# Kernel tuning notes

Hardware: AMD Instinct MI355X
Metric: run time of the kernel (lower is better)

Reference implementation:

```python
import jax, jax.numpy as jnp
import numpy as np

D_MODEL = 1024
N_HEADS = 16
HEAD_DIM = D_MODEL // N_HEADS


def setup_inputs() -> dict:
    key = jax.random.key(0)
    k1, k2, k3 = jax.random.split(key, 3)
    B, T = 2, 2048
    x = jax.random.normal(k1, (B, T, D_MODEL), dtype=jnp.float32)
    # causal lower-triangular mask; positions with mask==0 are blocked
    mask = jnp.tril(jnp.ones((T, T), dtype=jnp.int32))
    s = 1.0 / np.sqrt(D_MODEL)
    W_qkv = jax.random.normal(k2, (D_MODEL, 3 * D_MODEL), dtype=jnp.float32) * s
    W_out = jax.random.normal(k3, (D_MODEL, D_MODEL), dtype=jnp.float32) * s
    return {"x": x, "mask": mask, "W_qkv": W_qkv, "W_out": W_out}


def reference(x, mask, W_qkv, W_out):
    B, T, C = x.shape
    qkv = x @ W_qkv  # [B, T, 3C]
    q, k, v = jnp.split(qkv, 3, axis=-1)
    # [B, H, T, Dh]
    def heads(t):
        return t.reshape(B, T, N_HEADS, HEAD_DIM).transpose(0, 2, 1, 3)
    q, k, v = heads(q), heads(k), heads(v)
    scale = jnp.float32(1.0 / np.sqrt(HEAD_DIM))
    attn = jnp.einsum("bhqd,bhkd->bhqk", q, k) * scale  # [B,H,T,T]
    attn = jnp.where(mask == 0, jnp.float32(-jnp.inf), attn)
    attn = jax.nn.softmax(attn, axis=-1)
    out = jnp.einsum("bhqk,bhkd->bhqd", attn, v)  # [B,H,T,Dh]
    out = out.transpose(0, 2, 1, 3).reshape(B, T, C)
    return out @ W_out
```

## Files before the change

### kernel.cpp

```cpp
#include <hip/hip_runtime.h>
#include <hip/hip_bf16.h>

typedef __bf16 bf16;
typedef __bf16 bf16x4 __attribute__((ext_vector_type(4)));
typedef __bf16 bf16x8 __attribute__((ext_vector_type(8)));
typedef float f32x4 __attribute__((ext_vector_type(4)));
typedef float f32x16 __attribute__((ext_vector_type(16)));
typedef unsigned int uint4v __attribute__((ext_vector_type(4)));

__device__ __forceinline__ void gld_lds16(const void* g, void* l) {
  __builtin_amdgcn_global_load_lds(
      (const __attribute__((address_space(1))) void*)g,
      (__attribute__((address_space(3))) void*)l, 16, 0, 0);
}

__device__ __forceinline__ unsigned pkbf(float a, float b) {
  union { bf16 h[2]; unsigned u; } x;
  x.h[0] = (bf16)a; x.h[1] = (bf16)b;
  return x.u;
}

__device__ __forceinline__ void plswap2(unsigned& a, unsigned& b) {
  asm volatile("" : "+v"(a), "+v"(b));
  asm("v_permlane32_swap_b32 %0, %1" : "+v"(a), "+v"(b));
}

__device__ __forceinline__ float asf(unsigned u) { return __builtin_bit_cast(float, u); }

__device__ __forceinline__ float plsum(float x) {
  unsigned a = __builtin_bit_cast(unsigned, x), b = a;
  plswap2(a, b);
  return asf(a) + asf(b);
}

__global__ __launch_bounds__(256) void cvt_kernel(const float* __restrict__ src,
                                                  bf16* __restrict__ dst, int n4) {
  int i = blockIdx.x * 256 + threadIdx.x;
  if (i < n4) {
    float4 v = ((const float4*)src)[i];
    bf16x4 o = { (bf16)v.x, (bf16)v.y, (bf16)v.z, (bf16)v.w };
    ((bf16x4*)dst)[i] = o;
  }
}

__global__ __launch_bounds__(256) void transpose_cvt_kernel(const float* __restrict__ src,
                                                            bf16* __restrict__ dst,
                                                            int R, int C) {
  __shared__ float tile[32][33];
  int tx = threadIdx.x & 31, ty = threadIdx.x >> 5;
  int bx = blockIdx.x * 32, by = blockIdx.y * 32;
#pragma unroll
  for (int j = 0; j < 32; j += 8)
    tile[ty + j][tx] = src[(size_t)(by + ty + j) * C + bx + tx];
  __syncthreads();
#pragma unroll
  for (int j = 0; j < 32; j += 8)
    dst[(size_t)(bx + ty + j) * R + by + tx] = (bf16)tile[tx][ty + j];
}

__global__ __launch_bounds__(256) void transpose_v_kernel(const bf16* __restrict__ src,
                                                          bf16* __restrict__ dst) {
  __shared__ bf16 tile[32][34];
  int bh = blockIdx.z;
  int t0 = blockIdx.x * 32;
  int d0 = blockIdx.y * 32;
  int tx = threadIdx.x & 31, ty = threadIdx.x >> 5;
  const bf16* s = src + (size_t)bh * 2048 * 64;
  bf16* d = dst + (size_t)bh * 64 * 2048;
#pragma unroll
  for (int j = 0; j < 32; j += 8)
    tile[ty + j][tx] = s[(size_t)(t0 + ty + j) * 64 + d0 + tx];
  __syncthreads();
#pragma unroll
  for (int j = 0; j < 32; j += 8)
    d[(size_t)(d0 + ty + j) * 2048 + t0 + tx] = tile[tx][ty + j];
}

template <int MODE>
__global__ __launch_bounds__(256) void gemm_kernel(
    const bf16* __restrict__ A, const bf16* __restrict__ BT,
    float* __restrict__ Cf, bf16* __restrict__ qb, bf16* __restrict__ kb,
    bf16* __restrict__ vb, int M, int N, int K) {
  __shared__ bf16 As[128 * 64];
  __shared__ bf16 Bs[128 * 64];
  const int t = threadIdx.x;
  const int w = t >> 6, l = t & 63;

  int wid = blockIdx.y * gridDim.x + blockIdx.x;
  int cpx = (gridDim.x * gridDim.y) >> 3;
  int swz = (wid & 7) * cpx + (wid >> 3);
  const int bm = (swz / gridDim.x) * 128, bn = (swz % gridDim.x) * 128;

  const int wr = (w >> 1) * 64, wc = (w & 1) * 64;
  const int lr = l & 15, lh = l >> 4;
  f32x4 acc[4][4] = {};

  const bf16* Ab = A + (size_t)bm * K;
  const bf16* Bb = BT + (size_t)bn * K;
  char* AsB = (char*)As;
  char* BsB = (char*)Bs;

  const int srow_ = t >> 3;
  const int scol = (((t & 7) * 16) ^ ((srow_ & 7) << 4)) >> 1;
  const int ldsw = w * 1024;

  for (int k0 = 0; k0 < K; k0 += 64) {
    __syncthreads();
#pragma unroll
    for (int c = 0; c < 4; ++c) {
      const int row = c * 32 + srow_;
      gld_lds16(Ab + (size_t)row * K + k0 + scol, AsB + c * 4096 + ldsw);
      gld_lds16(Bb + (size_t)row * K + k0 + scol, BsB + c * 4096 + ldsw);
    }
    __syncthreads();
#pragma unroll
    for (int kk = 0; kk < 2; ++kk) {
      bf16x8 af[4], bfr[4];
#pragma unroll
      for (int m = 0; m < 4; ++m) {
        const int R = wr + m * 16 + lr;
        af[m] = *(const bf16x8*)(AsB + R * 128 + ((kk * 64 + lh * 16) ^ ((R & 7) << 4)));
      }
#pragma unroll
      for (int n = 0; n < 4; ++n) {
        const int R = wc + n * 16 + lr;
        bfr[n] = *(const bf16x8*)(BsB + R * 128 + ((kk * 64 + lh * 16) ^ ((R & 7) << 4)));
      }
#pragma unroll
      for (int m = 0; m < 4; ++m)
#pragma unroll
        for (int n = 0; n < 4; ++n)
          acc[m][n] = __builtin_amdgcn_mfma_f32_16x16x32_bf16(af[m], bfr[n],
                                                              acc[m][n], 0, 0, 0);
    }
  }

  const int r0 = bm + wr + (lh << 2);
  const int c0 = bn + wc + lr;
#pragma unroll
  for (int m = 0; m < 4; ++m) {
#pragma unroll
    for (int n = 0; n < 4; ++n) {
#pragma unroll
      for (int r = 0; r < 4; ++r) {
        float v = acc[m][n][r];
        int row = r0 + m * 16 + r;
        int col = c0 + n * 16;
        if (MODE == 2) {
          Cf[(size_t)row * N + col] = v;
        } else {
          int bb = row >> 11, tt = row & 2047;
          if (col < 1024) {
            int h = col >> 6, d = col & 63;
            qb[(((size_t)(bb * 16 + h)) * 2048 + tt) * 64 + d] = (bf16)v;
          } else if (col < 2048) {
            int c = col - 1024, h = c >> 6, d = c & 63;
            kb[(((size_t)(bb * 16 + h)) * 2048 + tt) * 64 + d] = (bf16)v;
          } else {
            int c = col - 2048, h = c >> 6, d = c & 63;
            vb[(((size_t)(bb * 16 + h)) * 2048 + tt) * 64 + d] = (bf16)v;
          }
        }
      }
    }
  }
}

template <bool FLIP>
__device__ __forceinline__ void attn_main(const bf16* __restrict__ Qh,
                                          const bf16* __restrict__ Kh,
                                          const bf16* __restrict__ Vh,
                                          bf16* __restrict__ ao,
                                          int qw, int lastkt, int l,
                                          int bb, int h, bf16 (*pl)[72]) {
  const int lq = l & 31, hi = l >> 5;
  const float sc2 = 0.125f * 1.4426950408889634f;

  bf16x8 qf[4];
#pragma unroll
  for (int c = 0; c < 4; ++c)
    qf[c] = *(const bf16x8*)(Qh + (size_t)(qw + lq) * 64 + c * 16 + hi * 8);

  f32x16 Ot0, Ot1;
#pragma unroll
  for (int r = 0; r < 16; ++r) { Ot0[r] = 0.f; Ot1[r] = 0.f; }
  float srun = 0.f;

  bf16x8 kA[4], vA[4], kB[4], vB[4];
#pragma unroll
  for (int c = 0; c < 4; ++c)
    kA[c] = *(const bf16x8*)(Kh + (size_t)lq * 64 + c * 16 + hi * 8);
#pragma unroll
  for (int df = 0; df < 2; ++df)
#pragma unroll
    for (int c = 0; c < 2; ++c)
      vA[df * 2 + c] = *(const bf16x8*)(Vh + (size_t)(df * 32 + lq) * 2048 + c * 16 + hi * 8);

  auto step = [&](bf16x8 (&KC)[4], bf16x8 (&VC)[4],
                  bf16x8 (&KN)[4], bf16x8 (&VN)[4], int kt) {
    const int nkv0 = (kt << 5) + 32;
#pragma unroll
    for (int c = 0; c < 4; ++c)
      KN[c] = *(const bf16x8*)(Kh + (size_t)(nkv0 + lq) * 64 + c * 16 + hi * 8);
#pragma unroll
    for (int df = 0; df < 2; ++df)
#pragma unroll
      for (int c = 0; c < 2; ++c)
        VN[df * 2 + c] = *(const bf16x8*)(Vh + (size_t)(df * 32 + lq) * 2048 + nkv0 + c * 16 + hi * 8);

    f32x16 S;
#pragma unroll
    for (int r = 0; r < 16; ++r) S[r] = 0.f;
#pragma unroll
    for (int c = 0; c < 4; ++c)
      S = __builtin_amdgcn_mfma_f32_32x32x16_bf16(KC[c], qf[c], S, 0, 0, 0);

    if (kt == lastkt) {
#pragma unroll
      for (int r = 0; r < 16; ++r) {
        int kvl = (r & 3) + 8 * (r >> 2) + 4 * hi;
        if (kvl > lq) S[r] = -1e30f;
      }
    }

    float ps = 0.f;
    unsigned u_[8];
#pragma unroll
    for (int i = 0; i < 8; ++i) {
      float pa = exp2f(S[2 * i] * sc2);
      float pb = exp2f(S[2 * i + 1] * sc2);
      ps += pa + pb;
      u_[i] = pkbf(pa, pb);
    }
    srun += plsum(ps);

    unsigned a0 = u_[0], b0 = u_[2]; plswap2(a0, b0);
    unsigned a1 = u_[1], b1 = u_[3]; plswap2(a1, b1);
    unsigned a2 = u_[4], b2 = u_[6]; plswap2(a2, b2);
    unsigned a3 = u_[5], b3 = u_[7]; plswap2(a3, b3);
    uint4v f0, f1;
    if (FLIP) { f0 = (uint4v){b0, b1, a0, a1}; f1 = (uint4v){b2, b3, a2, a3}; }
    else      { f0 = (uint4v){a0, a1, b0, b1}; f1 = (uint4v){a2, a3, b2, b3}; }
    bf16x8 pf0 = __builtin_bit_cast(bf16x8, f0);
    bf16x8 pf1 = __builtin_bit_cast(bf16x8, f1);

    Ot0 = __builtin_amdgcn_mfma_f32_32x32x16_bf16(VC[0], pf0, Ot0, 0, 0, 0);
    Ot0 = __builtin_amdgcn_mfma_f32_32x32x16_bf16(VC[1], pf1, Ot0, 0, 0, 0);
    Ot1 = __builtin_amdgcn_mfma_f32_32x32x16_bf16(VC[2], pf0, Ot1, 0, 0, 0);
    Ot1 = __builtin_amdgcn_mfma_f32_32x32x16_bf16(VC[3], pf1, Ot1, 0, 0, 0);
  };

  for (int kt = 0; kt <= lastkt; ++kt) {
    if ((kt & 1) == 0) step(kA, vA, kB, vB, kt);
    else               step(kB, vB, kA, vA, kt);
  }

  float inv = 1.0f / srun;
#pragma unroll
  for (int r = 0; r < 16; r += 2) {
    int d0 = (r & 3) + 8 * (r >> 2) + 4 * hi;
    *(unsigned*)&pl[lq][d0]      = pkbf(Ot0[r] * inv, Ot0[r + 1] * inv);
    *(unsigned*)&pl[lq][32 + d0] = pkbf(Ot1[r] * inv, Ot1[r + 1] * inv);
  }
  __builtin_amdgcn_s_waitcnt(0);

  const int q = l >> 1, dh = (l & 1) * 32;
  size_t orow = ((size_t)(bb * 2048 + qw + q)) * 1024 + h * 64 + dh;
#pragma unroll
  for (int c = 0; c < 4; ++c) {
    bf16x8 vv = *(const bf16x8*)&pl[q][dh + c * 8];
    *(bf16x8*)(ao + orow + c * 8) = vv;
  }
}

__global__ __launch_bounds__(512, 2) void attn_kernel(const bf16* __restrict__ qb,
                                                      const bf16* __restrict__ kb,
                                                      const bf16* __restrict__ vt,
                                                      bf16* __restrict__ ao) {
  __shared__ bf16 plds[8][32][72];
  int wid = blockIdx.y * 8 + blockIdx.x;
  int swz = (wid & 7) * 32 + (wid >> 3);
  const int bh = swz >> 3;
  const int grp = swz & 7;
  const int w = threadIdx.x >> 6, l = threadIdx.x & 63;
  const int jj = grp * 4 + (w & 3);
  const int qc = (w >> 2) ? (63 - jj) : jj;
  const bf16* Qh = qb + (size_t)bh * 2048 * 64;
  const bf16* Kh = kb + (size_t)bh * 2048 * 64;
  const bf16* Vh = vt + (size_t)bh * 64 * 2048;

  unsigned ta = (unsigned)l, tb = (unsigned)l;
  plswap2(ta, tb);
  const bool flipped = (ta != (unsigned)(l & 31));

  if (flipped)
    attn_main<true>(Qh, Kh, Vh, ao, qc * 32, qc, l, bh >> 4, bh & 15, plds[w]);
  else
    attn_main<false>(Qh, Kh, Vh, ao, qc * 32, qc, l, bh >> 4, bh & 15, plds[w]);
}

extern "C" void kernel_launch(void* const* d_in, const int* in_sizes, int n_in,
                              void* d_out, int out_size, void* d_ws, size_t ws_size,
                              hipStream_t stream) {
  const float* x = (const float*)d_in[0];
  const float* Wqkv = (const float*)d_in[2];
  const float* Wout = (const float*)d_in[3];
  float* out = (float*)d_out;

  char* ws = (char*)d_ws;
  bf16* xb  = (bf16*)(ws);
  bf16* wqT = (bf16*)(ws + (size_t)(8 << 20));
  bf16* woT = (bf16*)(ws + (size_t)(14 << 20));
  bf16* qb  = (bf16*)(ws + (size_t)(16 << 20));
  bf16* kb  = (bf16*)(ws + (size_t)(24 << 20));
  bf16* vt  = (bf16*)(ws + (size_t)(32 << 20));
  bf16* ao  = (bf16*)(ws + (size_t)(40 << 20));
  bf16* vb  = (bf16*)(ws + (size_t)(48 << 20));

  cvt_kernel<<<dim3(4096), dim3(256), 0, stream>>>(x, xb, 1048576);
  transpose_cvt_kernel<<<dim3(96, 32), dim3(256), 0, stream>>>(Wqkv, wqT, 1024, 3072);
  transpose_cvt_kernel<<<dim3(32, 32), dim3(256), 0, stream>>>(Wout, woT, 1024, 1024);
  gemm_kernel<1><<<dim3(24, 32), dim3(256), 0, stream>>>(xb, wqT, nullptr, qb, kb, vb,
                                                         4096, 3072, 1024);
  transpose_v_kernel<<<dim3(64, 2, 32), dim3(256), 0, stream>>>(vb, vt);
  attn_kernel<<<dim3(8, 32), dim3(512), 0, stream>>>(qb, kb, vt, ao);
  gemm_kernel<2><<<dim3(8, 32), dim3(256), 0, stream>>>(ao, woT, out, nullptr, nullptr,
                                                        nullptr, 4096, 1024, 1024);
}
```

Before: 219.3 us.

## Process two KV tiles per attention step with raw v_exp and MFMA priority

The attention inner loop now handles 64 keys per iteration, as two 32-key tiles, instead of 32. K for the next pair is prefetched into registers, while V is loaded at the start of the current step rather than one step ahead. The causal mask logic is rewritten to cover the two-tile pair, exp2f is replaced with inline v_exp_f32, and MFMA sections are wrapped in s_setprio. The aim is more instruction-level parallelism and fewer loop iterations, at the cost of higher register pressure and V loads that are exposed within the step.

```diff
diff --git a/kernel.cpp b/kernel.cpp
--- a/kernel.cpp
+++ b/kernel.cpp
@@ -18,6 +18,12 @@
   union { bf16 h[2]; unsigned u; } x;
   x.h[0] = (bf16)a; x.h[1] = (bf16)b;
   return x.u;
+}
+
+__device__ __forceinline__ float exp2r(float x) {
+  float r;
+  asm("v_exp_f32 %0, %1" : "=v"(r) : "v"(x));
+  return r;
 }
 
 __device__ __forceinline__ void plswap2(unsigned& a, unsigned& b) {
@@ -171,7 +177,7 @@
                                           const bf16* __restrict__ Kh,
                                           const bf16* __restrict__ Vh,
                                           bf16* __restrict__ ao,
-                                          int qw, int lastkt, int l,
+                                          int qw, int qc, int l,
                                           int bb, int h, bf16 (*pl)[72]) {
   const int lq = l & 31, hi = l >> 5;
   const float sc2 = 0.125f * 1.4426950408889634f;
@@ -186,73 +192,112 @@
   for (int r = 0; r < 16; ++r) { Ot0[r] = 0.f; Ot1[r] = 0.f; }
   float srun = 0.f;
 
-  bf16x8 kA[4], vA[4], kB[4], vB[4];
-#pragma unroll
-  for (int c = 0; c < 4; ++c)
-    kA[c] = *(const bf16x8*)(Kh + (size_t)lq * 64 + c * 16 + hi * 8);
-#pragma unroll
-  for (int df = 0; df < 2; ++df)
-#pragma unroll
-    for (int c = 0; c < 2; ++c)
-      vA[df * 2 + c] = *(const bf16x8*)(Vh + (size_t)(df * 32 + lq) * 2048 + c * 16 + hi * 8);
-
-  auto step = [&](bf16x8 (&KC)[4], bf16x8 (&VC)[4],
-                  bf16x8 (&KN)[4], bf16x8 (&VN)[4], int kt) {
-    const int nkv0 = (kt << 5) + 32;
+  bf16x8 kA[8], kB[8], vC[8];
+#pragma unroll
+  for (int tc = 0; tc < 8; ++tc)
+    kA[tc] = *(const bf16x8*)(Kh + (size_t)((tc >> 2) * 32 + lq) * 64 + (tc & 3) * 16 + hi * 8);
+
+  const int lastp = qc >> 1;
+
+  auto step = [&](bf16x8 (&KC)[8], bf16x8 (&KN)[8], int p) {
+    const int kv0 = p << 6;
+    const int nkv = kv0 + 64;
+#pragma unroll
+    for (int tc = 0; tc < 8; ++tc)
+      KN[tc] = *(const bf16x8*)(Kh + (size_t)(nkv + (tc >> 2) * 32 + lq) * 64 + (tc & 3) * 16 + hi * 8);
+#pragma unroll
+    for (int t = 0; t < 2; ++t)
+#pragma unroll
+      for (int df = 0; df < 2; ++df)
+#pragma unroll
+        for (int c = 0; c < 2; ++c)
+          vC[t * 4 + df * 2 + c] =
+              *(const bf16x8*)(Vh + (size_t)(df * 32 + lq) * 2048 + kv0 + t * 32 + c * 16 + hi * 8);
+
+    f32x16 S0, S1;
+#pragma unroll
+    for (int r = 0; r < 16; ++r) { S0[r] = 0.f; S1[r] = 0.f; }
+    __builtin_amdgcn_s_setprio(1);
 #pragma unroll
     for (int c = 0; c < 4; ++c)
-      KN[c] = *(const bf16x8*)(Kh + (size_t)(nkv0 + lq) * 64 + c * 16 + hi * 8);
-#pragma unroll
-    for (int df = 0; df < 2; ++df)
-#pragma unroll
-      for (int c = 0; c < 2; ++c)
-        VN[df * 2 + c] = *(const bf16x8*)(Vh + (size_t)(df * 32 + lq) * 2048 + nkv0 + c * 16 + hi * 8);
-
-    f32x16 S;
-#pragma unroll
-    for (int r = 0; r < 16; ++r) S[r] = 0.f;
+      S0 = __builtin_amdgcn_mfma_f32_32x32x16_bf16(KC[c], qf[c], S0, 0, 0, 0);
 #pragma unroll
     for (int c = 0; c < 4; ++c)
-      S = __builtin_amdgcn_mfma_f32_32x32x16_bf16(KC[c], qf[c], S, 0, 0, 0);
-
-    if (kt == lastkt) {
-#pragma unroll
-      for (int r = 0; r < 16; ++r) {
-        int kvl = (r & 3) + 8 * (r >> 2) + 4 * hi;
-        if (kvl > lq) S[r] = -1e30f;
+      S1 = __builtin_amdgcn_mfma_f32_32x32x16_bf16(KC[4 + c], qf[c], S1, 0, 0, 0);
+    __builtin_amdgcn_s_setprio(0);
+
+    const int t0 = 2 * p, t1 = 2 * p + 1;
+    if (t1 >= qc) {
+      if (t0 == qc) {
+#pragma unroll
+        for (int r = 0; r < 16; ++r) {
+          int kvl = (r & 3) + 8 * (r >> 2) + 4 * hi;
+          if (kvl > lq) S0[r] = -1e30f;
+          S1[r] = -1e30f;
+        }
+      } else {
+#pragma unroll
+        for (int r = 0; r < 16; ++r) {
+          int kvl = (r & 3) + 8 * (r >> 2) + 4 * hi;
+          if (kvl > lq) S1[r] = -1e30f;
+        }
       }
     }
 
-    float ps = 0.f;
-    unsigned u_[8];
+    float ps0 = 0.f, ps1 = 0.f;
+    unsigned u0_[8], u1_[8];
 #pragma unroll
     for (int i = 0; i < 8; ++i) {
-      float pa = exp2f(S[2 * i] * sc2);
-      float pb = exp2f(S[2 * i + 1] * sc2);
-      ps += pa + pb;
-      u_[i] = pkbf(pa, pb);
-    }
-    srun += plsum(ps);
-
-    unsigned a0 = u_[0], b0 = u_[2]; plswap2(a0, b0);
-    unsigned a1 = u_[1], b1 = u_[3]; plswap2(a1, b1);
-    unsigned a2 = u_[4], b2 = u_[6]; plswap2(a2, b2);
-    unsigned a3 = u_[5], b3 = u_[7]; plswap2(a3, b3);
-    uint4v f0, f1;
-    if (FLIP) { f0 = (uint4v){b0, b1, a0, a1}; f1 = (uint4v){b2, b3, a2, a3}; }
-    else      { f0 = (uint4v){a0, a1, b0, b1}; f1 = (uint4v){a2, a3, b2, b3}; }
-    bf16x8 pf0 = __builtin_bit_cast(bf16x8, f0);
-    bf16x8 pf1 = __builtin_bit_cast(bf16x8, f1);
-
-    Ot0 = __builtin_amdgcn_mfma_f32_32x32x16_bf16(VC[0], pf0, Ot0, 0, 0, 0);
-    Ot0 = __builtin_amdgcn_mfma_f32_32x32x16_bf16(VC[1], pf1, Ot0, 0, 0, 0);
-    Ot1 = __builtin_amdgcn_mfma_f32_32x32x16_bf16(VC[2], pf0, Ot1, 0, 0, 0);
-    Ot1 = __builtin_amdgcn_mfma_f32_32x32x16_bf16(VC[3], pf1, Ot1, 0, 0, 0);
+      float a = exp2r(S0[2 * i] * sc2);
+      float b = exp2r(S0[2 * i + 1] * sc2);
+      ps0 += a + b;
+      u0_[i] = pkbf(a, b);
+    }
+#pragma unroll
+    for (int i = 0; i < 8; ++i) {
+      float a = exp2r(S1[2 * i] * sc2);
+      float b = exp2r(S1[2 * i + 1] * sc2);
+      ps1 += a + b;
+      u1_[i] = pkbf(a, b);
+    }
+    srun += plsum(ps0 + ps1);
+
+    unsigned a0 = u0_[0], b0 = u0_[2]; plswap2(a0, b0);
+    unsigned a1 = u0_[1], b1 = u0_[3]; plswap2(a1, b1);
+    unsigned a2 = u0_[4], b2 = u0_[6]; plswap2(a2, b2);
+    unsigned a3 = u0_[5], b3 = u0_[7]; plswap2(a3, b3);
+    unsigned c0 = u1_[0], d0 = u1_[2]; plswap2(c0, d0);
+    unsigned c1 = u1_[1], d1 = u1_[3]; plswap2(c1, d1);
+    unsigned c2 = u1_[4], d2 = u1_[6]; plswap2(c2, d2);
+    unsigned c3 = u1_[5], d3 = u1_[7]; plswap2(c3, d3);
+    uint4v f00, f01, f10, f11;
+    if (FLIP) {
+      f00 = (uint4v){b0, b1, a0, a1}; f01 = (uint4v){b2, b3, a2, a3};
+      f10 = (uint4v){d0, d1, c0, c1}; f11 = (uint4v){d2, d3, c2, c3};
+    } else {
+      f00 = (uint4v){a0, a1, b0, b1}; f01 = (uint4v){a2, a3, b2, b3};
+      f10 = (uint4v){c0, c1, d0, d1}; f11 = (uint4v){c2, c3, d2, d3};
+    }
+    bf16x8 p00 = __builtin_bit_cast(bf16x8, f00);
+    bf16x8 p01 = __builtin_bit_cast(bf16x8, f01);
+    bf16x8 p10 = __builtin_bit_cast(bf16x8, f10);
+    bf16x8 p11 = __builtin_bit_cast(bf16x8, f11);
+
+    __builtin_amdgcn_s_setprio(1);
+    Ot0 = __builtin_amdgcn_mfma_f32_32x32x16_bf16(vC[0], p00, Ot0, 0, 0, 0);
+    Ot0 = __builtin_amdgcn_mfma_f32_32x32x16_bf16(vC[1], p01, Ot0, 0, 0, 0);
+    Ot1 = __builtin_amdgcn_mfma_f32_32x32x16_bf16(vC[2], p00, Ot1, 0, 0, 0);
+    Ot1 = __builtin_amdgcn_mfma_f32_32x32x16_bf16(vC[3], p01, Ot1, 0, 0, 0);
+    Ot0 = __builtin_amdgcn_mfma_f32_32x32x16_bf16(vC[4], p10, Ot0, 0, 0, 0);
+    Ot0 = __builtin_amdgcn_mfma_f32_32x32x16_bf16(vC[5], p11, Ot0, 0, 0, 0);
+    Ot1 = __builtin_amdgcn_mfma_f32_32x32x16_bf16(vC[6], p10, Ot1, 0, 0, 0);
+    Ot1 = __builtin_amdgcn_mfma_f32_32x32x16_bf16(vC[7], p11, Ot1, 0, 0, 0);
+    __builtin_amdgcn_s_setprio(0);
   };
 
-  for (int kt = 0; kt <= lastkt; ++kt) {
-    if ((kt & 1) == 0) step(kA, vA, kB, vB, kt);
-    else               step(kB, vB, kA, vA, kt);
+  for (int p = 0; p <= lastp; ++p) {
+    if ((p & 1) == 0) step(kA, kB, p);
+    else              step(kB, kA, p);
   }
 
   float inv = 1.0f / srun;
```

Measured after the change: 233.5 us. 6.5% more time.

## Software-pipeline QK^T one tile ahead of softmax/PV in attention loop

Applied to the files above, without the earlier changes.

Restructures the causal attention inner loop so the QK^T MFMA for the next key tile is issued before the exp/PV work of the current tile. K loads move two tiles ahead and V loads one tile ahead. It also brackets the MFMA groups with s_setprio and replaces exp2f with a raw v_exp_f32 inline asm. The aim is to overlap matrix-core work with the VALU exponentials and hide load latency, at the cost of more live registers. The final iteration computes an extra QK tile and issues loads past the causal range that are never used.

```diff
diff --git a/kernel.cpp b/kernel.cpp
--- a/kernel.cpp
+++ b/kernel.cpp
@@ -18,6 +18,12 @@
   union { bf16 h[2]; unsigned u; } x;
   x.h[0] = (bf16)a; x.h[1] = (bf16)b;
   return x.u;
+}
+
+__device__ __forceinline__ float exp2r(float x) {
+  float r;
+  asm("v_exp_f32 %0, %1" : "=v"(r) : "v"(x));
+  return r;
 }
 
 __device__ __forceinline__ void plswap2(unsigned& a, unsigned& b) {
@@ -171,7 +177,7 @@
                                           const bf16* __restrict__ Kh,
                                           const bf16* __restrict__ Vh,
                                           bf16* __restrict__ ao,
-                                          int qw, int lastkt, int l,
+                                          int qw, int qc, int l,
                                           int bb, int h, bf16 (*pl)[72]) {
   const int lq = l & 31, hi = l >> 5;
   const float sc2 = 0.125f * 1.4426950408889634f;
@@ -181,12 +187,12 @@
   for (int c = 0; c < 4; ++c)
     qf[c] = *(const bf16x8*)(Qh + (size_t)(qw + lq) * 64 + c * 16 + hi * 8);
 
-  f32x16 Ot0, Ot1;
+  f32x16 Ot0, Ot1, Sa, Sb;
 #pragma unroll
   for (int r = 0; r < 16; ++r) { Ot0[r] = 0.f; Ot1[r] = 0.f; }
   float srun = 0.f;
 
-  bf16x8 kA[4], vA[4], kB[4], vB[4];
+  bf16x8 kA[4], kB[4], vA[4], vB[4];
 #pragma unroll
   for (int c = 0; c < 4; ++c)
     kA[c] = *(const bf16x8*)(Kh + (size_t)lq * 64 + c * 16 + hi * 8);
@@ -195,31 +201,42 @@
 #pragma unroll
     for (int c = 0; c < 2; ++c)
       vA[df * 2 + c] = *(const bf16x8*)(Vh + (size_t)(df * 32 + lq) * 2048 + c * 16 + hi * 8);
-
-  auto step = [&](bf16x8 (&KC)[4], bf16x8 (&VC)[4],
-                  bf16x8 (&KN)[4], bf16x8 (&VN)[4], int kt) {
-    const int nkv0 = (kt << 5) + 32;
+#pragma unroll
+  for (int c = 0; c < 4; ++c)
+    kB[c] = *(const bf16x8*)(Kh + (size_t)(32 + lq) * 64 + c * 16 + hi * 8);
+#pragma unroll
+  for (int r = 0; r < 16; ++r) Sa[r] = 0.f;
+#pragma unroll
+  for (int c = 0; c < 4; ++c)
+    Sa = __builtin_amdgcn_mfma_f32_32x32x16_bf16(kA[c], qf[c], Sa, 0, 0, 0);
+
+  auto body = [&](f32x16& Scur, f32x16& Snext,
+                  bf16x8 (&Kq)[4], bf16x8 (&Kn)[4],
+                  bf16x8 (&Vc)[4], bf16x8 (&Vn)[4], int p) {
+    const int nkvK = (p + 2) << 5;
+    const int nkvV = (p + 1) << 5;
 #pragma unroll
     for (int c = 0; c < 4; ++c)
-      KN[c] = *(const bf16x8*)(Kh + (size_t)(nkv0 + lq) * 64 + c * 16 + hi * 8);
+      Kn[c] = *(const bf16x8*)(Kh + (size_t)(nkvK + lq) * 64 + c * 16 + hi * 8);
 #pragma unroll
     for (int df = 0; df < 2; ++df)
 #pragma unroll
       for (int c = 0; c < 2; ++c)
-        VN[df * 2 + c] = *(const bf16x8*)(Vh + (size_t)(df * 32 + lq) * 2048 + nkv0 + c * 16 + hi * 8);
-
-    f32x16 S;
-#pragma unroll
-    for (int r = 0; r < 16; ++r) S[r] = 0.f;
+        Vn[df * 2 + c] = *(const bf16x8*)(Vh + (size_t)(df * 32 + lq) * 2048 + nkvV + c * 16 + hi * 8);
+
+#pragma unroll
+    for (int r = 0; r < 16; ++r) Snext[r] = 0.f;
+    __builtin_amdgcn_s_setprio(1);
 #pragma unroll
     for (int c = 0; c < 4; ++c)
-      S = __builtin_amdgcn_mfma_f32_32x32x16_bf16(KC[c], qf[c], S, 0, 0, 0);
-
-    if (kt == lastkt) {
+      Snext = __builtin_amdgcn_mfma_f32_32x32x16_bf16(Kq[c], qf[c], Snext, 0, 0, 0);
+    __builtin_amdgcn_s_setprio(0);
+
+    if (p == qc) {
 #pragma unroll
       for (int r = 0; r < 16; ++r) {
         int kvl = (r & 3) + 8 * (r >> 2) + 4 * hi;
-        if (kvl > lq) S[r] = -1e30f;
+        if (kvl > lq) Scur[r] = -1e30f;
       }
     }
 
@@ -227,10 +244,10 @@
     unsigned u_[8];
 #pragma unroll
     for (int i = 0; i < 8; ++i) {
-      float pa = exp2f(S[2 * i] * sc2);
-      float pb = exp2f(S[2 * i + 1] * sc2);
-      ps += pa + pb;
-      u_[i] = pkbf(pa, pb);
+      float a = exp2r(Scur[2 * i] * sc2);
+      float b = exp2r(Scur[2 * i + 1] * sc2);
+      ps += a + b;
+      u_[i] = pkbf(a, b);
     }
     srun += plsum(ps);
 
@@ -244,15 +261,17 @@
     bf16x8 pf0 = __builtin_bit_cast(bf16x8, f0);
     bf16x8 pf1 = __builtin_bit_cast(bf16x8, f1);
 
-    Ot0 = __builtin_amdgcn_mfma_f32_32x32x16_bf16(VC[0], pf0, Ot0, 0, 0, 0);
-    Ot0 = __builtin_amdgcn_mfma_f32_32x32x16_bf16(VC[1], pf1, Ot0, 0, 0, 0);
-    Ot1 = __builtin_amdgcn_mfma_f32_32x32x16_bf16(VC[2], pf0, Ot1, 0, 0, 0);
-    Ot1 = __builtin_amdgcn_mfma_f32_32x32x16_bf16(VC[3], pf1, Ot1, 0, 0, 0);
+    __builtin_amdgcn_s_setprio(1);
+    Ot0 = __builtin_amdgcn_mfma_f32_32x32x16_bf16(Vc[0], pf0, Ot0, 0, 0, 0);
+    Ot0 = __builtin_amdgcn_mfma_f32_32x32x16_bf16(Vc[1], pf1, Ot0, 0, 0, 0);
+    Ot1 = __builtin_amdgcn_mfma_f32_32x32x16_bf16(Vc[2], pf0, Ot1, 0, 0, 0);
+    Ot1 = __builtin_amdgcn_mfma_f32_32x32x16_bf16(Vc[3], pf1, Ot1, 0, 0, 0);
+    __builtin_amdgcn_s_setprio(0);
   };
 
-  for (int kt = 0; kt <= lastkt; ++kt) {
-    if ((kt & 1) == 0) step(kA, vA, kB, vB, kt);
-    else               step(kB, vB, kA, vA, kt);
+  for (int p = 0; p <= qc; ++p) {
+    if ((p & 1) == 0) body(Sa, Sb, kB, kA, vA, vB, p);
+    else              body(Sb, Sa, kA, kB, vB, vA, p);
   }
 
   float inv = 1.0f / srun;
```

New measurement: 226.3 us. 1.03x slower.
